# Optimization experiments

Measured on AMD Instinct MI355X. Metric: run time of the kernel, lower is better.

The kernel has to match this reference:

```python
import jax, jax.numpy as jnp
import numpy as np

SEQ_LEN = 256
NLAYERS = 3
H = 128  # latent_dim == input_dim
OUT_DIM = 2
BATCH = 1024


def setup_inputs() -> dict:
    key = jax.random.key(0)
    ks = jax.random.split(key, 7)
    s = 1.0 / np.sqrt(H)  # PyTorch RNN init scale
    return {
        "hiddens": jax.random.normal(ks[0], (BATCH, NLAYERS, H), jnp.float32),
        "W_ih": jax.random.uniform(ks[1], (NLAYERS, 3 * H, H), jnp.float32, -s, s),
        "W_hh": jax.random.uniform(ks[2], (NLAYERS, 3 * H, H), jnp.float32, -s, s),
        "b_ih": jax.random.uniform(ks[3], (NLAYERS, 3 * H), jnp.float32, -s, s),
        "b_hh": jax.random.uniform(ks[4], (NLAYERS, 3 * H), jnp.float32, -s, s),
        "fc_w": jax.random.uniform(ks[5], (OUT_DIM, H), jnp.float32, -s, s),
        "fc_b": jax.random.uniform(ks[6], (OUT_DIM,), jnp.float32, -s, s),
    }


def _gru_cell(x, h, w_ih, w_hh, bi, bh):
    # x, h: [B, H]; w_*: [3H, H]; b_*: [3H]; PyTorch gate order (r, z, n)
    gx = x @ w_ih.T + bi          # [B, 3H]
    gh = h @ w_hh.T + bh          # [B, 3H]
    xr, xz, xn = jnp.split(gx, 3, axis=-1)
    hr, hz, hn = jnp.split(gh, 3, axis=-1)
    r = jax.nn.sigmoid(xr + hr)
    z = jax.nn.sigmoid(xz + hz)
    n = jnp.tanh(xn + r * hn)
    return (1.0 - z) * n + z * h


def reference(hiddens, W_ih, W_hh, b_ih, b_hh, fc_w, fc_b):
    # hiddens: [B, L, H] -> layer-major [L, B, H] (torch transposes 0,1)
    h = jnp.transpose(hiddens, (1, 0, 2))
    B = hiddens.shape[0]
    x0 = jnp.zeros((B, H), hiddens.dtype)  # torch.zeros initial input

    def step(carry, _):
        x, h = carry
        new_h = []
        inp = x
        for l in range(NLAYERS):
            hl = _gru_cell(inp, h[l], W_ih[l], W_hh[l], b_ih[l], b_hh[l])
            new_h.append(hl)
            inp = hl  # top-layer output feeds next layer / next step
        return (inp, jnp.stack(new_h)), inp

    (_, _), outs = jax.lax.scan(step, (x0, h), None, length=SEQ_LEN)
    outs = jnp.transpose(outs, (1, 0, 2))        # [B, T, H]
    return outs @ fc_w.T + fc_b                  # [B, T, out_dim]
```

## Files before the change

kernel.cpp:

```cpp
#include <hip/hip_runtime.h>
#include <stdint.h>

typedef int   v4i __attribute__((ext_vector_type(4)));
typedef float v4f __attribute__((ext_vector_type(4)));

#define SLOT_SZ  12288
#define LO_OFF   6144
#define BIAS_OFF (2*SLOT_SZ)
#define FC_OFF   (BIAS_OFF + 6144)
#define SMEM_SZ  (FC_OFF + 2048)

#define QW   1436.84056f
#define C1f  4.38394754e-5f
#define C2f  3.45193507e-7f
#define L2E  1.44269504f
#define CR1  (-(L2E)*C1f)
#define CR2  (-(L2E)*C2f)
#define CX1  (2.0f*L2E*C1f)
#define CX2  (2.0f*L2E*C2f)

#define MFMA(A,B,C) __builtin_amdgcn_mfma_i32_16x16x64_i8(A, B, C, 0, 0, 0)

__global__ void prep_weights(const float* __restrict__ Wih,
                             const float* __restrict__ Whh,
                             int8_t* __restrict__ img) {
  int bid = blockIdx.x, lane = threadIdx.x;
  int w = bid / 36, blk = bid % 36;
  int l = blk / 12, rem = blk % 12, o = rem >> 1, kh = rem & 1;
  const float* M = (o & 1) ? Whh : Wih;
  int row = (o >> 1) * 128 + w * 16 + (lane & 15);
  int k0 = kh * 64 + (lane >> 4) * 16;
  const float* src = M + l * 49152 + row * 128 + k0;
  int words[4];
  #pragma unroll
  for (int j4 = 0; j4 < 4; ++j4) {
    unsigned wd = 0;
    #pragma unroll
    for (int j = 0; j < 4; ++j) {
      int q = (int)rintf(src[j4 * 4 + j] * QW);
      wd |= ((unsigned)(q & 255)) << (8 * j);
    }
    words[j4] = (int)wd;
  }
  *(v4i*)(img + (((long)bid) * 64 + lane) * 16) = *(const v4i*)words;
}

#define DECL_ACC v4i aRh={0,0,0,0},aRl={0,0,0,0},aZh={0,0,0,0},aZl={0,0,0,0}, \
                     aXh={0,0,0,0},aXl={0,0,0,0},aHh={0,0,0,0},aHl={0,0,0,0}

#define HMFMA(L,H0,LL0,H1,LL1) do { \
  aRh = MFMA(wr[(L)*12+2],  H0,  aRh);  aRl = MFMA(wr[(L)*12+2],  LL0, aRl); \
  aZh = MFMA(wr[(L)*12+6],  H0,  aZh);  aZl = MFMA(wr[(L)*12+6],  LL0, aZl); \
  aHh = MFMA(wr[(L)*12+10], H0,  aHh);  aHl = MFMA(wr[(L)*12+10], LL0, aHl); \
  aRh = MFMA(wr[(L)*12+3],  H1,  aRh);  aRl = MFMA(wr[(L)*12+3],  LL1, aRl); \
  aZh = MFMA(wr[(L)*12+7],  H1,  aZh);  aZl = MFMA(wr[(L)*12+7],  LL1, aZl); \
  aHh = MFMA(wr[(L)*12+11], H1,  aHh);  aHl = MFMA(wr[(L)*12+11], LL1, aHl); \
} while(0)

#define XMFMA(L,H0,LL0,H1,LL1) do { \
  aRh = MFMA(wr[(L)*12+0],  H0,  aRh);  aRl = MFMA(wr[(L)*12+0],  LL0, aRl); \
  aZh = MFMA(wr[(L)*12+4],  H0,  aZh);  aZl = MFMA(wr[(L)*12+4],  LL0, aZl); \
  aXh = MFMA(wr[(L)*12+8],  H0,  aXh);  aXl = MFMA(wr[(L)*12+8],  LL0, aXl); \
  aRh = MFMA(wr[(L)*12+1],  H1,  aRh);  aRl = MFMA(wr[(L)*12+1],  LL1, aRl); \
  aZh = MFMA(wr[(L)*12+5],  H1,  aZh);  aZl = MFMA(wr[(L)*12+5],  LL1, aZl); \
  aXh = MFMA(wr[(L)*12+9],  H1,  aXh);  aXl = MFMA(wr[(L)*12+9],  LL1, aXl); \
} while(0)

#define EW_WRITE(L, SN, BR, BZ, BX, BH) do { \
  int hi_i[4], lo_i[4]; \
  _Pragma("unroll") \
  for (int r = 0; r < 4; ++r) { \
    float gR = fmaf(CR1, (float)aRh[r], fmaf(CR2, (float)aRl[r], (BR)[r])); \
    float gZ = fmaf(CR1, (float)aZh[r], fmaf(CR2, (float)aZl[r], (BZ)[r])); \
    float gX = fmaf(CX1, (float)aXh[r], fmaf(CX2, (float)aXl[r], (BX)[r])); \
    float gH = fmaf(CX1, (float)aHh[r], fmaf(CX2, (float)aHl[r], (BH)[r])); \
    float rg = __builtin_amdgcn_rcpf(1.f + __builtin_amdgcn_exp2f(gR)); \
    float zg = __builtin_amdgcn_rcpf(1.f + __builtin_amdgcn_exp2f(gZ)); \
    float u  = __builtin_amdgcn_rcpf(1.f + __builtin_amdgcn_exp2f(fmaf(rg, gH, gX))); \
    float ng = fmaf(-2.f, u, 1.f); \
    float hn = fmaf(zg, hst[L][r] - ng, ng); \
    hst[L][r] = hn; \
    float f = hn * 15.875f, fhi = rintf(f); \
    hi_i[r] = (int)fhi; \
    lo_i[r] = (int)rintf((f - fhi) * 127.f); \
  } \
  unsigned ph01 = __builtin_amdgcn_perm((unsigned)hi_i[1], (unsigned)hi_i[0], 0x00000400u); \
  unsigned ph23 = __builtin_amdgcn_perm((unsigned)hi_i[3], (unsigned)hi_i[2], 0x04000000u); \
  unsigned hiw  = __builtin_amdgcn_perm(ph23, ph01, 0x07060100u); \
  unsigned pl01 = __builtin_amdgcn_perm((unsigned)lo_i[1], (unsigned)lo_i[0], 0x00000400u); \
  unsigned pl23 = __builtin_amdgcn_perm((unsigned)lo_i[3], (unsigned)lo_i[2], 0x04000000u); \
  unsigned low  = __builtin_amdgcn_perm(pl23, pl01, 0x07060100u); \
  *(unsigned*)(ewb + (SN) + (L)*2048)          = hiw; \
  *(unsigned*)(ewb + (SN) + (L)*2048 + LO_OFF) = low; \
} while(0)

__global__ __launch_bounds__(512, 1)
void gru_main(const float* __restrict__ hiddens, const float* __restrict__ bih,
              const float* __restrict__ bhh, const float* __restrict__ fcw,
              const float* __restrict__ fcb, const int8_t* __restrict__ img,
              float* __restrict__ out) {
  extern __shared__ char smem[];
  const int tid = threadIdx.x, wg = blockIdx.x;
  const int lane = tid & 63, w = tid >> 6, col = lane & 15, q = lane >> 4;

  v4i wr[36];
  #pragma unroll
  for (int i = 0; i < 36; ++i)
    wr[i] = *(const v4i*)(img + (((long)(w * 36 + i)) * 64 + lane) * 16);

  if (tid < 128) {
    int kh = tid >> 6, ln = tid & 63, c2 = ln & 15, q2 = ln >> 4;
    int words[4] = {0, 0, 0, 0};
    if (c2 < 2) {
      const float* src = fcw + c2 * 128 + kh * 64 + q2 * 16;
      #pragma unroll
      for (int j4 = 0; j4 < 4; ++j4) {
        unsigned wd = 0;
        #pragma unroll
        for (int j = 0; j < 4; ++j) {
          int qv = (int)rintf(src[j4 * 4 + j] * QW);
          wd |= ((unsigned)(qv & 255)) << (8 * j);
        }
        words[j4] = (int)wd;
      }
    }
    *(v4i*)(smem + FC_OFF + kh * 1024 + ln * 16) = *(const v4i*)words;
  }
  for (int i = tid; i < 1536; i += 512) {
    int l = i >> 9, type = (i >> 7) & 3, h = i & 127;
    float bv;
    if      (type == 0) bv = -L2E * (bih[l * 384 + h]       + bhh[l * 384 + h]);
    else if (type == 1) bv = -L2E * (bih[l * 384 + 128 + h] + bhh[l * 384 + 128 + h]);
    else if (type == 2) bv = 2.0f * L2E * bih[l * 384 + 256 + h];
    else                bv = 2.0f * L2E * bhh[l * 384 + 256 + h];
    *(float*)(smem + BIAS_OFF + i * 4) = bv;
  }
  for (int i = tid; i < 6144; i += 512) {
    int l = i >> 11, b = (i >> 7) & 15, h = i & 127;
    float v = hiddens[((long)(wg * 16 + b)) * 384 + l * 128 + h];
    float f = v * 15.875f, fhi = rintf(f);
    int addr = l * 2048 + (h >> 4) * 256 + b * 16 + (h & 15);
    *(int8_t*)(smem + addr)          = (int8_t)(int)fhi;
    *(int8_t*)(smem + addr + LO_OFF) = (int8_t)(int)rintf((f - fhi) * 127.f);
  }
  v4f hst[3];
  #pragma unroll
  for (int l = 0; l < 3; ++l)
    #pragma unroll
    for (int r = 0; r < 4; ++r)
      hst[l][r] = hiddens[((long)(wg * 16 + col)) * 384 + l * 128 + w * 16 + q * 4 + r];

  const float fcb0 = fcb[0], fcb1 = fcb[1];
  __syncthreads();

  const char* fragb = smem + lane * 16;
  char* ewb = smem + w * 256 + col * 16 + q * 4;
  const char* biasb = smem + BIAS_OFF + (w * 16 + q * 4) * 4;

  v4i Ah0 = *(const v4i*)(fragb + 0);
  v4i Al0 = *(const v4i*)(fragb + 0 + LO_OFF);
  v4i Ah1 = *(const v4i*)(fragb + 1024);
  v4i Al1 = *(const v4i*)(fragb + 1024 + LO_OFF);
  v4i Bh0 = *(const v4i*)(fragb + 2048);
  v4i Bl0 = *(const v4i*)(fragb + 2048 + LO_OFF);
  v4i Bh1 = *(const v4i*)(fragb + 2048 + 1024);
  v4i Bl1 = *(const v4i*)(fragb + 2048 + 1024 + LO_OFF);
  v4i Ch0, Cl0, Ch1, Cl1;

  #pragma unroll 1
  for (int t = 0; t < 256; ++t) {
    const int so = (t & 1) * SLOT_SZ;
    const int sn = SLOT_SZ - so;

    {
      DECL_ACC;
      Ch0 = *(const v4i*)(fragb + so + 2 * 2048);
      Cl0 = *(const v4i*)(fragb + so + 2 * 2048 + LO_OFF);
      Ch1 = *(const v4i*)(fragb + so + 2 * 2048 + 1024);
      Cl1 = *(const v4i*)(fragb + so + 2 * 2048 + 1024 + LO_OFF);
      v4f bRv = *(const v4f*)(biasb + 0 * 512);
      v4f bZv = *(const v4f*)(biasb + 1 * 512);
      v4f bXv = *(const v4f*)(biasb + 2 * 512);
      v4f bHv = *(const v4f*)(biasb + 3 * 512);
      HMFMA(0, Ah0, Al0, Ah1, Al1);
      if (t > 0) {
        XMFMA(0, Ch0, Cl0, Ch1, Cl1);
        if (w == 0) {
          v4i dh = {0,0,0,0}, dl = {0,0,0,0};
          v4i fwA = *(const v4i*)(smem + FC_OFF + 0 * 1024 + lane * 16);
          v4i fwB = *(const v4i*)(smem + FC_OFF + 1 * 1024 + lane * 16);
          dh = MFMA(fwA, Ch0, dh);  dl = MFMA(fwA, Cl0, dl);
          dh = MFMA(fwB, Ch1, dh);  dl = MFMA(fwB, Cl1, dl);
          if (q == 0) {
            float2 o2;
            o2.x = fcb0 + C1f * (float)dh[0] + C2f * (float)dl[0];
            o2.y = fcb1 + C1f * (float)dh[1] + C2f * (float)dl[1];
            *(float2*)(out + (((long)(wg * 16 + col)) * 256 + (t - 1)) * 2) = o2;
          }
        }
      }
      EW_WRITE(0, sn, bRv, bZv, bXv, bHv);
      __syncthreads();
    }
    {
      DECL_ACC;
      Ah0 = *(const v4i*)(fragb + sn + 0);
      Al0 = *(const v4i*)(fragb + sn + 0 + LO_OFF);
      Ah1 = *(const v4i*)(fragb + sn + 1024);
      Al1 = *(const v4i*)(fragb + sn + 1024 + LO_OFF);
      v4f bRv = *(const v4f*)(biasb + 4 * 512);
      v4f bZv = *(const v4f*)(biasb + 5 * 512);
      v4f bXv = *(const v4f*)(biasb + 6 * 512);
      v4f bHv = *(const v4f*)(biasb + 7 * 512);
      HMFMA(1, Bh0, Bl0, Bh1, Bl1);
      XMFMA(1, Ah0, Al0, Ah1, Al1);
      EW_WRITE(1, sn, bRv, bZv, bXv, bHv);
      __syncthreads();
    }
    {
      DECL_ACC;
      Bh0 = *(const v4i*)(fragb + sn + 2048);
      Bl0 = *(const v4i*)(fragb + sn + 2048 + LO_OFF);
      Bh1 = *(const v4i*)(fragb + sn + 2048 + 1024);
      Bl1 = *(const v4i*)(fragb + sn + 2048 + 1024 + LO_OFF);
      v4f bRv = *(const v4f*)(biasb + 8 * 512);
      v4f bZv = *(const v4f*)(biasb + 9 * 512);
      v4f bXv = *(const v4f*)(biasb + 10 * 512);
      v4f bHv = *(const v4f*)(biasb + 11 * 512);
      HMFMA(2, Ch0, Cl0, Ch1, Cl1);
      XMFMA(2, Bh0, Bl0, Bh1, Bl1);
      EW_WRITE(2, sn, bRv, bZv, bXv, bHv);
      __syncthreads();
    }
  }
  if (w == 0) {
    v4i dh = {0,0,0,0}, dl = {0,0,0,0};
    v4i xh0 = *(const v4i*)(fragb + 2 * 2048);
    v4i xl0 = *(const v4i*)(fragb + 2 * 2048 + LO_OFF);
    v4i xh1 = *(const v4i*)(fragb + 2 * 2048 + 1024);
    v4i xl1 = *(const v4i*)(fragb + 2 * 2048 + 1024 + LO_OFF);
    v4i fwA = *(const v4i*)(smem + FC_OFF + 0 * 1024 + lane * 16);
    v4i fwB = *(const v4i*)(smem + FC_OFF + 1 * 1024 + lane * 16);
    dh = MFMA(fwA, xh0, dh);  dl = MFMA(fwA, xl0, dl);
    dh = MFMA(fwB, xh1, dh);  dl = MFMA(fwB, xl1, dl);
    if (q == 0) {
      float2 o2;
      o2.x = fcb0 + C1f * (float)dh[0] + C2f * (float)dl[0];
      o2.y = fcb1 + C1f * (float)dh[1] + C2f * (float)dl[1];
      *(float2*)(out + (((long)(wg * 16 + col)) * 256 + 255) * 2) = o2;
    }
  }
}

extern "C" void kernel_launch(void* const* d_in, const int* in_sizes, int n_in,
                              void* d_out, int out_size, void* d_ws, size_t ws_size,
                              hipStream_t stream) {
  (void)in_sizes; (void)n_in; (void)out_size; (void)ws_size;
  const float* hiddens = (const float*)d_in[0];
  const float* Wih     = (const float*)d_in[1];
  const float* Whh     = (const float*)d_in[2];
  const float* bih     = (const float*)d_in[3];
  const float* bhh     = (const float*)d_in[4];
  const float* fcw     = (const float*)d_in[5];
  const float* fcb     = (const float*)d_in[6];
  int8_t* img = (int8_t*)d_ws;
  float* out = (float*)d_out;

  prep_weights<<<288, 64, 0, stream>>>(Wih, Whh, img);
  gru_main<<<64, 512, SMEM_SZ, stream>>>(hiddens, bih, bhh, fcw, fcb, img, out);
}
```

Before: 756.7 us.

## Software-pipeline recurrent h-projection MFMAs one stage ahead with double accumulator sets

The step loop is unrolled by two so that slot offsets become compile-time constants. Two accumulator sets now alternate, so the hidden-to-hidden MFMAs for the next layer stage are issued before the current stage's input MFMAs and elementwise gate math. This lets the recurrent matmul, which only needs state from the previous step, overlap with the latency of the dependent chain across each barrier. It roughly doubles accumulator register pressure with launch bounds fixed at 512 threads, so spilling is a risk.

```diff
diff --git a/kernel.cpp b/kernel.cpp
--- a/kernel.cpp
+++ b/kernel.cpp
@@ -45,35 +45,41 @@
   *(v4i*)(img + (((long)bid) * 64 + lane) * 16) = *(const v4i*)words;
 }
 
-#define DECL_ACC v4i aRh={0,0,0,0},aRl={0,0,0,0},aZh={0,0,0,0},aZl={0,0,0,0}, \
-                     aXh={0,0,0,0},aXl={0,0,0,0},aHh={0,0,0,0},aHl={0,0,0,0}
-
-#define HMFMA(L,H0,LL0,H1,LL1) do { \
-  aRh = MFMA(wr[(L)*12+2],  H0,  aRh);  aRl = MFMA(wr[(L)*12+2],  LL0, aRl); \
-  aZh = MFMA(wr[(L)*12+6],  H0,  aZh);  aZl = MFMA(wr[(L)*12+6],  LL0, aZl); \
-  aHh = MFMA(wr[(L)*12+10], H0,  aHh);  aHl = MFMA(wr[(L)*12+10], LL0, aHl); \
-  aRh = MFMA(wr[(L)*12+3],  H1,  aRh);  aRl = MFMA(wr[(L)*12+3],  LL1, aRl); \
-  aZh = MFMA(wr[(L)*12+7],  H1,  aZh);  aZl = MFMA(wr[(L)*12+7],  LL1, aZl); \
-  aHh = MFMA(wr[(L)*12+11], H1,  aHh);  aHl = MFMA(wr[(L)*12+11], LL1, aHl); \
+#define DECL_SET(S) v4i S##Rh=z4,S##Rl=z4,S##Zh=z4,S##Zl=z4, \
+                        S##Xh=z4,S##Xl=z4,S##Hh=z4,S##Hl=z4
+#define ZERO_SET(S) do { S##Rh=z4;S##Rl=z4;S##Zh=z4;S##Zl=z4; \
+                         S##Xh=z4;S##Xl=z4;S##Hh=z4;S##Hl=z4; } while(0)
+
+#define HMFMA_S(S,L,H0,LL0,H1,LL1) do { \
+  S##Rh = MFMA(wr[(L)*12+2],  H0,  S##Rh);  S##Rl = MFMA(wr[(L)*12+2],  LL0, S##Rl); \
+  S##Zh = MFMA(wr[(L)*12+6],  H0,  S##Zh);  S##Zl = MFMA(wr[(L)*12+6],  LL0, S##Zl); \
+  S##Hh = MFMA(wr[(L)*12+10], H0,  S##Hh);  S##Hl = MFMA(wr[(L)*12+10], LL0, S##Hl); \
+  S##Rh = MFMA(wr[(L)*12+3],  H1,  S##Rh);  S##Rl = MFMA(wr[(L)*12+3],  LL1, S##Rl); \
+  S##Zh = MFMA(wr[(L)*12+7],  H1,  S##Zh);  S##Zl = MFMA(wr[(L)*12+7],  LL1, S##Zl); \
+  S##Hh = MFMA(wr[(L)*12+11], H1,  S##Hh);  S##Hl = MFMA(wr[(L)*12+11], LL1, S##Hl); \
 } while(0)
 
-#define XMFMA(L,H0,LL0,H1,LL1) do { \
-  aRh = MFMA(wr[(L)*12+0],  H0,  aRh);  aRl = MFMA(wr[(L)*12+0],  LL0, aRl); \
-  aZh = MFMA(wr[(L)*12+4],  H0,  aZh);  aZl = MFMA(wr[(L)*12+4],  LL0, aZl); \
-  aXh = MFMA(wr[(L)*12+8],  H0,  aXh);  aXl = MFMA(wr[(L)*12+8],  LL0, aXl); \
-  aRh = MFMA(wr[(L)*12+1],  H1,  aRh);  aRl = MFMA(wr[(L)*12+1],  LL1, aRl); \
-  aZh = MFMA(wr[(L)*12+5],  H1,  aZh);  aZl = MFMA(wr[(L)*12+5],  LL1, aZl); \
-  aXh = MFMA(wr[(L)*12+9],  H1,  aXh);  aXl = MFMA(wr[(L)*12+9],  LL1, aXl); \
+#define XMFMA_S(S,L,H0,LL0,H1,LL1) do { \
+  S##Rh = MFMA(wr[(L)*12+0],  H0,  S##Rh);  S##Rl = MFMA(wr[(L)*12+0],  LL0, S##Rl); \
+  S##Zh = MFMA(wr[(L)*12+4],  H0,  S##Zh);  S##Zl = MFMA(wr[(L)*12+4],  LL0, S##Zl); \
+  S##Xh = MFMA(wr[(L)*12+8],  H0,  S##Xh);  S##Xl = MFMA(wr[(L)*12+8],  LL0, S##Xl); \
+  S##Rh = MFMA(wr[(L)*12+1],  H1,  S##Rh);  S##Rl = MFMA(wr[(L)*12+1],  LL1, S##Rl); \
+  S##Zh = MFMA(wr[(L)*12+5],  H1,  S##Zh);  S##Zl = MFMA(wr[(L)*12+5],  LL1, S##Zl); \
+  S##Xh = MFMA(wr[(L)*12+9],  H1,  S##Xh);  S##Xl = MFMA(wr[(L)*12+9],  LL1, S##Xl); \
 } while(0)
 
-#define EW_WRITE(L, SN, BR, BZ, BX, BH) do { \
+#define EW_S(S, L, SN) do { \
+  v4f bRv = *(const v4f*)(biasb + ((L)*4 + 0) * 512); \
+  v4f bZv = *(const v4f*)(biasb + ((L)*4 + 1) * 512); \
+  v4f bXv = *(const v4f*)(biasb + ((L)*4 + 2) * 512); \
+  v4f bHv = *(const v4f*)(biasb + ((L)*4 + 3) * 512); \
   int hi_i[4], lo_i[4]; \
   _Pragma("unroll") \
   for (int r = 0; r < 4; ++r) { \
-    float gR = fmaf(CR1, (float)aRh[r], fmaf(CR2, (float)aRl[r], (BR)[r])); \
-    float gZ = fmaf(CR1, (float)aZh[r], fmaf(CR2, (float)aZl[r], (BZ)[r])); \
-    float gX = fmaf(CX1, (float)aXh[r], fmaf(CX2, (float)aXl[r], (BX)[r])); \
-    float gH = fmaf(CX1, (float)aHh[r], fmaf(CX2, (float)aHl[r], (BH)[r])); \
+    float gR = fmaf(CR1, (float)S##Rh[r], fmaf(CR2, (float)S##Rl[r], bRv[r])); \
+    float gZ = fmaf(CR1, (float)S##Zh[r], fmaf(CR2, (float)S##Zl[r], bZv[r])); \
+    float gX = fmaf(CX1, (float)S##Xh[r], fmaf(CX2, (float)S##Xl[r], bXv[r])); \
+    float gH = fmaf(CX1, (float)S##Hh[r], fmaf(CX2, (float)S##Hl[r], bHv[r])); \
     float rg = __builtin_amdgcn_rcpf(1.f + __builtin_amdgcn_exp2f(gR)); \
     float zg = __builtin_amdgcn_rcpf(1.f + __builtin_amdgcn_exp2f(gZ)); \
     float u  = __builtin_amdgcn_rcpf(1.f + __builtin_amdgcn_exp2f(fmaf(rg, gH, gX))); \
@@ -94,6 +100,20 @@
   *(unsigned*)(ewb + (SN) + (L)*2048 + LO_OFF) = low; \
 } while(0)
 
+#define FC_EMIT(TIDX) do { if (w == 0) { \
+  v4i dh = z4, dl = z4; \
+  v4i fwA = *(const v4i*)(smem + FC_OFF + 0 * 1024 + lane * 16); \
+  v4i fwB = *(const v4i*)(smem + FC_OFF + 1 * 1024 + lane * 16); \
+  dh = MFMA(fwA, Ch0, dh);  dl = MFMA(fwA, Cl0, dl); \
+  dh = MFMA(fwB, Ch1, dh);  dl = MFMA(fwB, Cl1, dl); \
+  if (q == 0) { \
+    float2 o2; \
+    o2.x = fcb0 + C1f * (float)dh[0] + C2f * (float)dl[0]; \
+    o2.y = fcb1 + C1f * (float)dh[1] + C2f * (float)dl[1]; \
+    *(float2*)(out + (((long)(wg * 16 + col)) * 256 + (TIDX)) * 2) = o2; \
+  } \
+} } while(0)
+
 __global__ __launch_bounds__(512, 1)
 void gru_main(const float* __restrict__ hiddens, const float* __restrict__ bih,
               const float* __restrict__ bhh, const float* __restrict__ fcw,
@@ -102,6 +122,7 @@
   extern __shared__ char smem[];
   const int tid = threadIdx.x, wg = blockIdx.x;
   const int lane = tid & 63, w = tid >> 6, col = lane & 15, q = lane >> 4;
+  const v4i z4 = {0, 0, 0, 0};
 
   v4i wr[36];
   #pragma unroll
@@ -167,74 +188,85 @@
   v4i Bl1 = *(const v4i*)(fragb + 2048 + 1024 + LO_OFF);
   v4i Ch0, Cl0, Ch1, Cl1;
 
+  DECL_SET(P);
+  DECL_SET(Q);
+  HMFMA_S(P, 0, Ah0, Al0, Ah1, Al1);
+
   #pragma unroll 1
-  for (int t = 0; t < 256; ++t) {
-    const int so = (t & 1) * SLOT_SZ;
-    const int sn = SLOT_SZ - so;
-
-    {
-      DECL_ACC;
-      Ch0 = *(const v4i*)(fragb + so + 2 * 2048);
-      Cl0 = *(const v4i*)(fragb + so + 2 * 2048 + LO_OFF);
-      Ch1 = *(const v4i*)(fragb + so + 2 * 2048 + 1024);
-      Cl1 = *(const v4i*)(fragb + so + 2 * 2048 + 1024 + LO_OFF);
-      v4f bRv = *(const v4f*)(biasb + 0 * 512);
-      v4f bZv = *(const v4f*)(biasb + 1 * 512);
-      v4f bXv = *(const v4f*)(biasb + 2 * 512);
-      v4f bHv = *(const v4f*)(biasb + 3 * 512);
-      HMFMA(0, Ah0, Al0, Ah1, Al1);
+  for (int t = 0; t < 256; t += 2) {
+    {
+      Ch0 = *(const v4i*)(fragb + 0 + 2 * 2048);
+      Cl0 = *(const v4i*)(fragb + 0 + 2 * 2048 + LO_OFF);
+      Ch1 = *(const v4i*)(fragb + 0 + 2 * 2048 + 1024);
+      Cl1 = *(const v4i*)(fragb + 0 + 2 * 2048 + 1024 + LO_OFF);
+      ZERO_SET(Q);
+      HMFMA_S(Q, 1, Bh0, Bl0, Bh1, Bl1);
       if (t > 0) {
-        XMFMA(0, Ch0, Cl0, Ch1, Cl1);
-        if (w == 0) {
-          v4i dh = {0,0,0,0}, dl = {0,0,0,0};
-          v4i fwA = *(const v4i*)(smem + FC_OFF + 0 * 1024 + lane * 16);
-          v4i fwB = *(const v4i*)(smem + FC_OFF + 1 * 1024 + lane * 16);
-          dh = MFMA(fwA, Ch0, dh);  dl = MFMA(fwA, Cl0, dl);
-          dh = MFMA(fwB, Ch1, dh);  dl = MFMA(fwB, Cl1, dl);
-          if (q == 0) {
-            float2 o2;
-            o2.x = fcb0 + C1f * (float)dh[0] + C2f * (float)dl[0];
-            o2.y = fcb1 + C1f * (float)dh[1] + C2f * (float)dl[1];
-            *(float2*)(out + (((long)(wg * 16 + col)) * 256 + (t - 1)) * 2) = o2;
-          }
-        }
+        XMFMA_S(P, 0, Ch0, Cl0, Ch1, Cl1);
+        FC_EMIT(t - 1);
       }
-      EW_WRITE(0, sn, bRv, bZv, bXv, bHv);
-      __syncthreads();
-    }
-    {
-      DECL_ACC;
-      Ah0 = *(const v4i*)(fragb + sn + 0);
-      Al0 = *(const v4i*)(fragb + sn + 0 + LO_OFF);
-      Ah1 = *(const v4i*)(fragb + sn + 1024);
-      Al1 = *(const v4i*)(fragb + sn + 1024 + LO_OFF);
-      v4f bRv = *(const v4f*)(biasb + 4 * 512);
-      v4f bZv = *(const v4f*)(biasb + 5 * 512);
-      v4f bXv = *(const v4f*)(biasb + 6 * 512);
-      v4f bHv = *(const v4f*)(biasb + 7 * 512);
-      HMFMA(1, Bh0, Bl0, Bh1, Bl1);
-      XMFMA(1, Ah0, Al0, Ah1, Al1);
-      EW_WRITE(1, sn, bRv, bZv, bXv, bHv);
-      __syncthreads();
-    }
-    {
-      DECL_ACC;
-      Bh0 = *(const v4i*)(fragb + sn + 2048);
-      Bl0 = *(const v4i*)(fragb + sn + 2048 + LO_OFF);
-      Bh1 = *(const v4i*)(fragb + sn + 2048 + 1024);
-      Bl1 = *(const v4i*)(fragb + sn + 2048 + 1024 + LO_OFF);
-      v4f bRv = *(const v4f*)(biasb + 8 * 512);
-      v4f bZv = *(const v4f*)(biasb + 9 * 512);
-      v4f bXv = *(const v4f*)(biasb + 10 * 512);
-      v4f bHv = *(const v4f*)(biasb + 11 * 512);
-      HMFMA(2, Ch0, Cl0, Ch1, Cl1);
-      XMFMA(2, Bh0, Bl0, Bh1, Bl1);
-      EW_WRITE(2, sn, bRv, bZv, bXv, bHv);
+      EW_S(P, 0, SLOT_SZ);
+      __syncthreads();
+    }
+    {
+      Ah0 = *(const v4i*)(fragb + SLOT_SZ + 0);
+      Al0 = *(const v4i*)(fragb + SLOT_SZ + 0 + LO_OFF);
+      Ah1 = *(const v4i*)(fragb + SLOT_SZ + 1024);
+      Al1 = *(const v4i*)(fragb + SLOT_SZ + 1024 + LO_OFF);
+      ZERO_SET(P);
+      HMFMA_S(P, 2, Ch0, Cl0, Ch1, Cl1);
+      XMFMA_S(Q, 1, Ah0, Al0, Ah1, Al1);
+      EW_S(Q, 1, SLOT_SZ);
+      __syncthreads();
+    }
+    {
+      Bh0 = *(const v4i*)(fragb + SLOT_SZ + 2048);
+      Bl0 = *(const v4i*)(fragb + SLOT_SZ + 2048 + LO_OFF);
+      Bh1 = *(const v4i*)(fragb + SLOT_SZ + 2048 + 1024);
+      Bl1 = *(const v4i*)(fragb + SLOT_SZ + 2048 + 1024 + LO_OFF);
+      ZERO_SET(Q);
+      HMFMA_S(Q, 0, Ah0, Al0, Ah1, Al1);
+      XMFMA_S(P, 2, Bh0, Bl0, Bh1, Bl1);
+      EW_S(P, 2, SLOT_SZ);
+      __syncthreads();
+    }
+    {
+      Ch0 = *(const v4i*)(fragb + SLOT_SZ + 2 * 2048);
+      Cl0 = *(const v4i*)(fragb + SLOT_SZ + 2 * 2048 + LO_OFF);
+      Ch1 = *(const v4i*)(fragb + SLOT_SZ + 2 * 2048 + 1024);
+      Cl1 = *(const v4i*)(fragb + SLOT_SZ + 2 * 2048 + 1024 + LO_OFF);
+      ZERO_SET(P);
+      HMFMA_S(P, 1, Bh0, Bl0, Bh1, Bl1);
+      XMFMA_S(Q, 0, Ch0, Cl0, Ch1, Cl1);
+      FC_EMIT(t);
+      EW_S(Q, 0, 0);
+      __syncthreads();
+    }
+    {
+      Ah0 = *(const v4i*)(fragb + 0);
+      Al0 = *(const v4i*)(fragb + 0 + LO_OFF);
+      Ah1 = *(const v4i*)(fragb + 1024);
+      Al1 = *(const v4i*)(fragb + 1024 + LO_OFF);
+      ZERO_SET(Q);
+      HMFMA_S(Q, 2, Ch0, Cl0, Ch1, Cl1);
+      XMFMA_S(P, 1, Ah0, Al0, Ah1, Al1);
+      EW_S(P, 1, 0);
+      __syncthreads();
+    }
+    {
+      Bh0 = *(const v4i*)(fragb + 2048);
+      Bl0 = *(const v4i*)(fragb + 2048 + LO_OFF);
+      Bh1 = *(const v4i*)(fragb + 2048 + 1024);
+      Bl1 = *(const v4i*)(fragb + 2048 + 1024 + LO_OFF);
+      ZERO_SET(P);
+      HMFMA_S(P, 0, Ah0, Al0, Ah1, Al1);
+      XMFMA_S(Q, 2, Bh0, Bl0, Bh1, Bl1);
+      EW_S(Q, 2, 0);
       __syncthreads();
     }
   }
   if (w == 0) {
-    v4i dh = {0,0,0,0}, dl = {0,0,0,0};
+    v4i dh = z4, dl = z4;
     v4i xh0 = *(const v4i*)(fragb + 2 * 2048);
     v4i xl0 = *(const v4i*)(fragb + 2 * 2048 + LO_OFF);
     v4i xh1 = *(const v4i*)(fragb + 2 * 2048 + 1024);
```

Result: slower. 800.7 us (+5.8%).
